# Kernel tuning notes

Measured on AMD Instinct MI355X. Metric: run time of the kernel, lower is better.

## Reference

```python
import jax, jax.numpy as jnp
import numpy as np

N_NODES = 25000
N_EDGES = 400000
N = 2          # per-node group dim (h.size(1))
IN_DIM = 64
HEADS = 4
HEAD_DIM = 16  # out_dim; HEADS*HEAD_DIM == IN_DIM here


def setup_inputs() -> dict:
    key = jax.random.key(0)
    ks = jax.random.split(key, 8)
    w_scale = 1.0 / np.sqrt(IN_DIM)
    return {
        "h": jax.random.normal(ks[0], (N_NODES, N, IN_DIM), jnp.float32),
        "e": jax.random.normal(ks[1], (N_EDGES, N, IN_DIM), jnp.float32),
        "W_Q": jax.random.normal(ks[2], (IN_DIM, HEADS * HEAD_DIM), jnp.float32) * w_scale,
        "W_K": jax.random.normal(ks[3], (IN_DIM, HEADS * HEAD_DIM), jnp.float32) * w_scale,
        "W_V": jax.random.normal(ks[4], (IN_DIM, HEADS * HEAD_DIM), jnp.float32) * w_scale,
        "W_repe": jax.random.normal(ks[5], (IN_DIM, HEADS * HEAD_DIM), jnp.float32) * w_scale,
        "src": jax.random.randint(ks[6], (N_EDGES,), 0, N_NODES, jnp.int32),
        "dst": jax.random.randint(ks[7], (N_EDGES,), 0, N_NODES, jnp.int32),
    }


def reference(h, e, W_Q, W_K, W_V, W_repe, src, dst):
    n_nodes, Nd, C = h.shape
    E = src.shape[0]
    # node-side projection Q_h: [n_nodes, N, H, D]
    Q_h = (h @ W_Q).reshape(n_nodes, Nd, HEADS, HEAD_DIM)
    # edge-side bias repe_e: [E, N, H, D]
    repe_e = (e @ W_repe).reshape(E, Nd, HEADS, HEAD_DIM)
    # compute_diff: relu(src - dst) on raw features  [E, N, C]
    diff = jax.nn.relu(h[src] - h[dst])
    k_diff = (diff @ W_K).reshape(E, Nd, HEADS, HEAD_DIM)
    v_diff = (diff @ W_V).reshape(E, Nd, HEADS, HEAD_DIM)
    # dst_cosim_diff: scale = ||k_diff|| * ||Q_h[dst]|| + 1e-6 (norm over last dim, keepdim)
    q_dst = Q_h[dst]  # [E, N, H, D]
    scale = (jnp.linalg.norm(k_diff, axis=-1, keepdims=True)
             * jnp.linalg.norm(q_dst, axis=-1, keepdims=True)) + 1e-6
    score = q_dst * k_diff * scale + repe_e
    msg = score * v_diff
    # update_all(copy_edge, max) -> segment max over dst; zero-degree nodes get 0 (DGL convention)
    h_out = jax.ops.segment_max(msg, dst, num_segments=n_nodes)
    h_out = jnp.where(jnp.isneginf(h_out), jnp.zeros((), h_out.dtype), h_out)
    return h_out
```

## Files before the change

kernel.cpp:

```cpp
#include <hip/hip_runtime.h>
#include <stdint.h>

#define N_NODES 25000
#define N_EDGES 400000

typedef __attribute__((ext_vector_type(8))) short short8;
typedef __attribute__((ext_vector_type(4))) float f32x4;

#define MFMA16(a, b, c) __builtin_amdgcn_mfma_f32_16x16x32_bf16((a), (b), (c), 0, 0, 0)

__device__ __forceinline__ short bf16r(float x) {
    unsigned u = __float_as_uint(x);
    u += 0x7FFFu + ((u >> 16) & 1u);
    return (short)(u >> 16);
}
__device__ __forceinline__ short bfr(float x) {
    return (short)((__float_as_uint(x) + 0x8000u) >> 16);
}

#define DPP_ADD(x, ctrl) \
    ((x) + __int_as_float(__builtin_amdgcn_update_dpp(0, __float_as_int(x), (ctrl), 0xF, 0xF, true)))
__device__ __forceinline__ float red16(float x) {
    x = DPP_ADD(x, 0xB1);
    x = DPP_ADD(x, 0x4E);
    x = DPP_ADD(x, 0x141);
    x = DPP_ADD(x, 0x140);
    return x;
}

__device__ __forceinline__ short8 load_bfrag(const float* __restrict__ W,
                                             int colbase, int lane, int khalf) {
    const int n = colbase + (lane & 15);
    const int k0 = khalf * 32 + ((lane >> 4) << 3);
    short8 f;
    #pragma unroll
    for (int j = 0; j < 8; ++j) f[j] = bf16r(W[(k0 + j) * 64 + n]);
    return f;
}

__device__ __forceinline__ short8 afrag(const short* S, int lane, int khalf) {
    return *(const short8*)&S[(lane & 15) * 72 + khalf * 32 + ((lane >> 4) << 3)];
}

__global__ __launch_bounds__(256) void zero_counts_kernel(int* __restrict__ counts) {
    const int i = blockIdx.x * 256 + threadIdx.x;
    if (i < N_NODES) counts[i] = 0;
}

__global__ __launch_bounds__(256) void hist_kernel(const int* __restrict__ dst,
                                                   int* __restrict__ counts) {
    const int i = blockIdx.x * 256 + threadIdx.x;
    if (i < N_EDGES) atomicAdd(&counts[dst[i]], 1);
}

#define BPT 98
__global__ __launch_bounds__(256) void scan_kernel(const int* __restrict__ counts,
                                                   int* __restrict__ offsets,
                                                   int* __restrict__ cursor) {
    __shared__ int part[256];
    const int t = threadIdx.x;
    const int base = t * BPT;
    int s = 0;
    for (int j = 0; j < BPT; ++j) {
        const int idx = base + j;
        if (idx < N_NODES) s += counts[idx];
    }
    part[t] = s;
    __syncthreads();
    for (int d = 1; d < 256; d <<= 1) {
        const int add = (t >= d) ? part[t - d] : 0;
        __syncthreads();
        part[t] += add;
        __syncthreads();
    }
    int run = (t > 0) ? part[t - 1] : 0;
    for (int j = 0; j < BPT; ++j) {
        const int idx = base + j;
        if (idx < N_NODES) {
            offsets[idx] = run;
            cursor[idx]  = run;
            run += counts[idx];
        }
    }
    if (t == 255) offsets[N_NODES] = part[255];
}

__global__ __launch_bounds__(256) void scatter_pos_kernel(
    const int* __restrict__ dst, int* __restrict__ cursor,
    int* __restrict__ csr_pos) {
    const int i = blockIdx.x * 256 + threadIdx.x;
    if (i < N_EDGES) {
        const int pos = atomicAdd(&cursor[dst[i]], 1);
        csr_pos[i] = pos;
    }
}

__global__ __launch_bounds__(256) void q_mfma_kernel(
    const float* __restrict__ h, const float* __restrict__ Wq,
    const float* __restrict__ Wk, const float* __restrict__ Wv,
    const float* __restrict__ Wr, float* __restrict__ Q, short8* __restrict__ fw)
{
    __shared__ short sH[64 * 72];
    const int t = threadIdx.x;
    const int lane = t & 63, w = t >> 6;
    const int wcol = w << 4;
    const int ln = lane & 15, lq = lane >> 4;
    const int base = blockIdx.x * 64;

    const short8 b0 = load_bfrag(Wq, wcol, lane, 0);
    const short8 b1 = load_bfrag(Wq, wcol, lane, 1);

    {
        const int r = t >> 2, c4 = (t & 3) << 4;
        int row = base + r; if (row > 49999) row = 49999;
        const float4* p = (const float4*)&h[row * 64 + c4];
        short tmp[16];
        #pragma unroll
        for (int i = 0; i < 4; ++i) {
            float4 x = p[i];
            tmp[4*i+0] = bf16r(x.x); tmp[4*i+1] = bf16r(x.y);
            tmp[4*i+2] = bf16r(x.z); tmp[4*i+3] = bf16r(x.w);
        }
        *(short8*)&sH[r * 72 + c4]     = *(short8*)&tmp[0];
        *(short8*)&sH[r * 72 + c4 + 8] = *(short8*)&tmp[8];
    }
    __syncthreads();

    #pragma unroll
    for (int m = 0; m < 4; ++m) {
        const short* Sm = &sH[(m << 4) * 72];
        short8 a0 = afrag(Sm, lane, 0);
        short8 a1 = afrag(Sm, lane, 1);
        f32x4 acc = {0.f, 0.f, 0.f, 0.f};
        acc = MFMA16(a0, b0, acc);
        acc = MFMA16(a1, b1, acc);
        #pragma unroll
        for (int reg = 0; reg < 4; ++reg) {
            const float qn = sqrtf(red16(acc[reg] * acc[reg]));
            const int row = base + (m << 4) + (lq << 2) + reg;
            if (row < 50000) Q[row * 64 + wcol + ln] = acc[reg] * qn;
        }
    }

    if (blockIdx.x == 0) {
        fw[(w * 6 + 0) * 64 + lane] = load_bfrag(Wk, wcol, lane, 0);
        fw[(w * 6 + 1) * 64 + lane] = load_bfrag(Wk, wcol, lane, 1);
        fw[(w * 6 + 2) * 64 + lane] = load_bfrag(Wv, wcol, lane, 0);
        fw[(w * 6 + 3) * 64 + lane] = load_bfrag(Wv, wcol, lane, 1);
        fw[(w * 6 + 4) * 64 + lane] = load_bfrag(Wr, wcol, lane, 0);
        fw[(w * 6 + 5) * 64 + lane] = load_bfrag(Wr, wcol, lane, 1);
    }
}

__global__ __launch_bounds__(256, 4) void edge_msg_kernel(
    const float* __restrict__ h, const float* __restrict__ e,
    const float* __restrict__ QQ, const int* __restrict__ src,
    const int* __restrict__ dst, const int* __restrict__ csr_pos,
    const short8* __restrict__ fw, uint2* __restrict__ msg)
{
    const int t = threadIdx.x;
    const int lane = t & 63;
    const int g = (blockIdx.x << 2) + (t >> 6);
    const int g8 = g << 3;
    const int ln = lane & 15, lq = lane >> 4;
    const int eloc = ln >> 1, nr = ln & 1;
    const int k0 = lq << 3;

    const int sA = src[g8 + eloc];
    const int dA = dst[g8 + eloc];
    const float* __restrict__ hs  = &h[((sA << 1) + nr) << 6];
    const float* __restrict__ hdp = &h[((dA << 1) + nr) << 6];
    const float* __restrict__ ep  = &e[(((g8 + eloc) << 1) + nr) << 6];

    short8 afr[2], gfr[2];
    #pragma unroll
    for (int half = 0; half < 2; ++half) {
        const int cb = (half << 5) + k0;
        const float4 s0 = *(const float4*)&hs[cb];
        const float4 s1 = *(const float4*)&hs[cb + 4];
        const float4 d0 = *(const float4*)&hdp[cb];
        const float4 d1 = *(const float4*)&hdp[cb + 4];
        const float4 e0 = *(const float4*)&ep[cb];
        const float4 e1 = *(const float4*)&ep[cb + 4];
        short8 ta, tg;
        ta[0] = bfr(fmaxf(s0.x - d0.x, 0.f));
        ta[1] = bfr(fmaxf(s0.y - d0.y, 0.f));
        ta[2] = bfr(fmaxf(s0.z - d0.z, 0.f));
        ta[3] = bfr(fmaxf(s0.w - d0.w, 0.f));
        ta[4] = bfr(fmaxf(s1.x - d1.x, 0.f));
        ta[5] = bfr(fmaxf(s1.y - d1.y, 0.f));
        ta[6] = bfr(fmaxf(s1.z - d1.z, 0.f));
        ta[7] = bfr(fmaxf(s1.w - d1.w, 0.f));
        tg[0] = bfr(e0.x); tg[1] = bfr(e0.y); tg[2] = bfr(e0.z); tg[3] = bfr(e0.w);
        tg[4] = bfr(e1.x); tg[5] = bfr(e1.y); tg[6] = bfr(e1.z); tg[7] = bfr(e1.w);
        afr[half] = ta;
        gfr[half] = tg;
    }

    const int e0i = g8 + (lq << 1), e1i = e0i + 1;
    const int d0 = dst[e0i], d1 = dst[e1i];
    const int p0 = csr_pos[e0i], p1 = csr_pos[e1i];

    float qv_e0n0[4], qv_e0n1[4], qv_e1n0[4], qv_e1n1[4];
    #pragma unroll
    for (int hd = 0; hd < 4; ++hd) {
        qv_e0n0[hd] = QQ[(d0 << 7) + (hd << 4) + ln];
        qv_e0n1[hd] = QQ[(d0 << 7) + 64 + (hd << 4) + ln];
        qv_e1n0[hd] = QQ[(d1 << 7) + (hd << 4) + ln];
        qv_e1n1[hd] = QQ[(d1 << 7) + 64 + (hd << 4) + ln];
    }

    f32x4 aK[4], aV[4], aR[4];
    #pragma unroll
    for (int hd = 0; hd < 4; ++hd) {
        f32x4 k = {0.f, 0.f, 0.f, 0.f}, vv = k, r = k;
        k  = MFMA16(afr[0], fw[(hd * 6 + 0) * 64 + lane], k);
        k  = MFMA16(afr[1], fw[(hd * 6 + 1) * 64 + lane], k);
        vv = MFMA16(afr[0], fw[(hd * 6 + 2) * 64 + lane], vv);
        vv = MFMA16(afr[1], fw[(hd * 6 + 3) * 64 + lane], vv);
        r  = MFMA16(gfr[0], fw[(hd * 6 + 4) * 64 + lane], r);
        r  = MFMA16(gfr[1], fw[(hd * 6 + 5) * 64 + lane], r);
        aK[hd] = k; aV[hd] = vv; aR[hd] = r;
    }

    #pragma unroll
    for (int reg = 0; reg < 4; ++reg) {
        float m[4];
        #pragma unroll
        for (int hd = 0; hd < 4; ++hd) {
            const float kk = aK[hd][reg];
            const float nk = sqrtf(red16(kk * kk));
            const float qv = (reg == 0) ? qv_e0n0[hd] :
                             (reg == 1) ? qv_e0n1[hd] :
                             (reg == 2) ? qv_e1n0[hd] : qv_e1n1[hd];
            m[hd] = (qv * kk * nk + aR[hd][reg]) * aV[hd][reg];
        }
        uint2 pk;
        pk.x = (unsigned)(unsigned short)bf16r(m[0])
             | ((unsigned)(unsigned short)bf16r(m[1]) << 16);
        pk.y = (unsigned)(unsigned short)bf16r(m[2])
             | ((unsigned)(unsigned short)bf16r(m[3]) << 16);
        const int p = (reg & 2) ? p1 : p0;
        msg[(((p << 1) + (reg & 1)) << 4) + ln] = pk;
    }
}

__global__ __launch_bounds__(256) void reduce_kernel(
    const unsigned* __restrict__ msg_u, const int* __restrict__ offsets,
    float* __restrict__ out)
{
    const int t = threadIdx.x;
    const int lane = t & 63;
    const int v = (blockIdx.x << 2) + (t >> 6);
    const int off0 = offsets[v], off1 = offsets[v + 1];
    const int n = lane >> 5, ph = (lane >> 4) & 1, ln = lane & 15;
    const unsigned* __restrict__ p = msg_u + ((n << 5) + (ln << 1) + ph);

    const float NEG_INF = __uint_as_float(0xFF800000u);
    float m0 = NEG_INF, m1 = NEG_INF;

    int pos = off0;
    for (; pos + 4 <= off1; pos += 4) {
        const unsigned u0 = p[(pos + 0) << 6];
        const unsigned u1 = p[(pos + 1) << 6];
        const unsigned u2 = p[(pos + 2) << 6];
        const unsigned u3 = p[(pos + 3) << 6];
        m0 = fmaxf(m0, __uint_as_float(u0 << 16));
        m1 = fmaxf(m1, __uint_as_float(u0 & 0xFFFF0000u));
        m0 = fmaxf(m0, __uint_as_float(u1 << 16));
        m1 = fmaxf(m1, __uint_as_float(u1 & 0xFFFF0000u));
        m0 = fmaxf(m0, __uint_as_float(u2 << 16));
        m1 = fmaxf(m1, __uint_as_float(u2 & 0xFFFF0000u));
        m0 = fmaxf(m0, __uint_as_float(u3 << 16));
        m1 = fmaxf(m1, __uint_as_float(u3 & 0xFFFF0000u));
    }
    for (; pos < off1; ++pos) {
        const unsigned u = p[pos << 6];
        m0 = fmaxf(m0, __uint_as_float(u << 16));
        m1 = fmaxf(m1, __uint_as_float(u & 0xFFFF0000u));
    }
    if (off0 == off1) { m0 = 0.f; m1 = 0.f; }

    const int col = (n << 6) + (ph << 5) + ln;
    out[(v << 7) + col]      = m0;
    out[(v << 7) + col + 16] = m1;
}

extern "C" void kernel_launch(void* const* d_in, const int* in_sizes, int n_in,
                              void* d_out, int out_size, void* d_ws, size_t ws_size,
                              hipStream_t stream) {
    const float* h  = (const float*)d_in[0];
    const float* e  = (const float*)d_in[1];
    const float* Wq = (const float*)d_in[2];
    const float* Wk = (const float*)d_in[3];
    const float* Wv = (const float*)d_in[4];
    const float* Wr = (const float*)d_in[5];
    const int*   src = (const int*)d_in[6];
    const int*   dst = (const int*)d_in[7];
    float* out = (float*)d_out;

    float* Q       = (float*)d_ws;
    int*   counts  = (int*)d_ws + 3200000;
    int*   offsets = (int*)d_ws + 3225000;
    int*   cursor  = (int*)d_ws + 3250008;
    int*   csr_pos = (int*)d_ws + 3275008;
    short8* fw     = (short8*)((int*)d_ws + 3675008);
    uint2* msg     = (uint2*)((int*)d_ws + 3681152);

    zero_counts_kernel<<<98, 256, 0, stream>>>(counts);
    hist_kernel<<<1563, 256, 0, stream>>>(dst, counts);
    scan_kernel<<<1, 256, 0, stream>>>(counts, offsets, cursor);
    scatter_pos_kernel<<<1563, 256, 0, stream>>>(dst, cursor, csr_pos);
    q_mfma_kernel<<<782, 256, 0, stream>>>(h, Wq, Wk, Wv, Wr, Q, fw);
    edge_msg_kernel<<<12500, 256, 0, stream>>>(h, e, Q, src, dst, csr_pos, fw, msg);
    reduce_kernel<<<6250, 256, 0, stream>>>((const unsigned*)msg, offsets, out);
}
```

Before: 534.9 us.

## Replace CSR segment-max with atomicMax on order-mapped floats and bf16 node buffer

```diff
diff --git a/kernel.cpp b/kernel.cpp
--- a/kernel.cpp
+++ b/kernel.cpp
@@ -28,6 +28,25 @@
     return x;
 }
 
+__device__ __forceinline__ unsigned fmap(float x) {
+    const unsigned u = __float_as_uint(x);
+    return ((int)u >= 0) ? (u | 0x80000000u) : ~u;
+}
+#define MAPPED_NEG_INF 0x007FFFFFu
+
+__device__ __forceinline__ float pickbf(unsigned u, int odd) {
+    return __uint_as_float(odd ? (u & 0xFFFF0000u) : (u << 16));
+}
+__device__ __forceinline__ unsigned drelu_pack(unsigned s, unsigned d) {
+    const float slo = __uint_as_float(s << 16);
+    const float shi = __uint_as_float(s & 0xFFFF0000u);
+    const float dlo = __uint_as_float(d << 16);
+    const float dhi = __uint_as_float(d & 0xFFFF0000u);
+    const unsigned lo = (unsigned short)bfr(fmaxf(slo - dlo, 0.f));
+    const unsigned hi = (unsigned short)bfr(fmaxf(shi - dhi, 0.f));
+    return lo | (hi << 16);
+}
+
 __device__ __forceinline__ short8 load_bfrag(const float* __restrict__ W,
                                              int colbase, int lane, int khalf) {
     const int n = colbase + (lane & 15);
@@ -42,63 +61,15 @@
     return *(const short8*)&S[(lane & 15) * 72 + khalf * 32 + ((lane >> 4) << 3)];
 }
 
-__global__ __launch_bounds__(256) void zero_counts_kernel(int* __restrict__ counts) {
+__global__ __launch_bounds__(256) void init_kernel(unsigned* __restrict__ out_u) {
     const int i = blockIdx.x * 256 + threadIdx.x;
-    if (i < N_NODES) counts[i] = 0;
-}
-
-__global__ __launch_bounds__(256) void hist_kernel(const int* __restrict__ dst,
-                                                   int* __restrict__ counts) {
-    const int i = blockIdx.x * 256 + threadIdx.x;
-    if (i < N_EDGES) atomicAdd(&counts[dst[i]], 1);
-}
-
-#define BPT 98
-__global__ __launch_bounds__(256) void scan_kernel(const int* __restrict__ counts,
-                                                   int* __restrict__ offsets,
-                                                   int* __restrict__ cursor) {
-    __shared__ int part[256];
-    const int t = threadIdx.x;
-    const int base = t * BPT;
-    int s = 0;
-    for (int j = 0; j < BPT; ++j) {
-        const int idx = base + j;
-        if (idx < N_NODES) s += counts[idx];
-    }
-    part[t] = s;
-    __syncthreads();
-    for (int d = 1; d < 256; d <<= 1) {
-        const int add = (t >= d) ? part[t - d] : 0;
-        __syncthreads();
-        part[t] += add;
-        __syncthreads();
-    }
-    int run = (t > 0) ? part[t - 1] : 0;
-    for (int j = 0; j < BPT; ++j) {
-        const int idx = base + j;
-        if (idx < N_NODES) {
-            offsets[idx] = run;
-            cursor[idx]  = run;
-            run += counts[idx];
-        }
-    }
-    if (t == 255) offsets[N_NODES] = part[255];
-}
-
-__global__ __launch_bounds__(256) void scatter_pos_kernel(
-    const int* __restrict__ dst, int* __restrict__ cursor,
-    int* __restrict__ csr_pos) {
-    const int i = blockIdx.x * 256 + threadIdx.x;
-    if (i < N_EDGES) {
-        const int pos = atomicAdd(&cursor[dst[i]], 1);
-        csr_pos[i] = pos;
-    }
+    out_u[i] = MAPPED_NEG_INF;
 }
 
 __global__ __launch_bounds__(256) void q_mfma_kernel(
     const float* __restrict__ h, const float* __restrict__ Wq,
     const float* __restrict__ Wk, const float* __restrict__ Wv,
-    const float* __restrict__ Wr, float* __restrict__ Q, short8* __restrict__ fw)
+    const float* __restrict__ Wr, unsigned* __restrict__ NB, short8* __restrict__ fw)
 {
     __shared__ short sH[64 * 72];
     const int t = threadIdx.x;
@@ -123,6 +94,9 @@
         }
         *(short8*)&sH[r * 72 + c4]     = *(short8*)&tmp[0];
         *(short8*)&sH[r * 72 + c4 + 8] = *(short8*)&tmp[8];
+        unsigned* nb = NB + ((row >> 1) << 7) + ((row & 1) << 5) + (c4 >> 1);
+        *(short8*)(nb)     = *(short8*)&tmp[0];
+        *(short8*)(nb + 4) = *(short8*)&tmp[8];
     }
     __syncthreads();
 
@@ -137,8 +111,14 @@
         #pragma unroll
         for (int reg = 0; reg < 4; ++reg) {
             const float qn = sqrtf(red16(acc[reg] * acc[reg]));
+            const float qq = acc[reg] * qn;
+            const float qo = __shfl_xor(qq, 1);
             const int row = base + (m << 4) + (lq << 2) + reg;
-            if (row < 50000) Q[row * 64 + wcol + ln] = acc[reg] * qn;
+            if (((ln & 1) == 0) && row < 50000) {
+                const unsigned u = (unsigned)(unsigned short)bf16r(qq)
+                                 | ((unsigned)(unsigned short)bf16r(qo) << 16);
+                NB[((row >> 1) << 7) + 64 + ((row & 1) << 5) + (w << 3) + (ln >> 1)] = u;
+            }
         }
     }
 
@@ -152,11 +132,10 @@
     }
 }
 
-__global__ __launch_bounds__(256, 4) void edge_msg_kernel(
-    const float* __restrict__ h, const float* __restrict__ e,
-    const float* __restrict__ QQ, const int* __restrict__ src,
-    const int* __restrict__ dst, const int* __restrict__ csr_pos,
-    const short8* __restrict__ fw, uint2* __restrict__ msg)
+__global__ __launch_bounds__(256, 4) void edge_atomic_kernel(
+    const float* __restrict__ e, const int* __restrict__ src,
+    const int* __restrict__ dst, const unsigned* __restrict__ NB,
+    const short8* __restrict__ fw, unsigned* __restrict__ out_u)
 {
     const int t = threadIdx.x;
     const int lane = t & 63;
@@ -168,122 +147,88 @@
 
     const int sA = src[g8 + eloc];
     const int dA = dst[g8 + eloc];
-    const float* __restrict__ hs  = &h[((sA << 1) + nr) << 6];
-    const float* __restrict__ hdp = &h[((dA << 1) + nr) << 6];
-    const float* __restrict__ ep  = &e[(((g8 + eloc) << 1) + nr) << 6];
-
-    short8 afr[2], gfr[2];
+    const unsigned* nbs = NB + (sA << 7) + (nr << 5);
+    const unsigned* nbd = NB + (dA << 7) + (nr << 5);
+    const uint4 su0 = ((const uint4*)nbs)[lq];
+    const uint4 su1 = ((const uint4*)nbs)[4 + lq];
+    const uint4 du0 = ((const uint4*)nbd)[lq];
+    const uint4 du1 = ((const uint4*)nbd)[4 + lq];
+    uint4 a0u, a1u;
+    a0u.x = drelu_pack(su0.x, du0.x); a0u.y = drelu_pack(su0.y, du0.y);
+    a0u.z = drelu_pack(su0.z, du0.z); a0u.w = drelu_pack(su0.w, du0.w);
+    a1u.x = drelu_pack(su1.x, du1.x); a1u.y = drelu_pack(su1.y, du1.y);
+    a1u.z = drelu_pack(su1.z, du1.z); a1u.w = drelu_pack(su1.w, du1.w);
+    const short8 afr0 = *(const short8*)&a0u;
+    const short8 afr1 = *(const short8*)&a1u;
+
+    const float* __restrict__ ep = &e[(((g8 + eloc) << 1) + nr) << 6];
+    short8 gfr0, gfr1;
     #pragma unroll
     for (int half = 0; half < 2; ++half) {
         const int cb = (half << 5) + k0;
-        const float4 s0 = *(const float4*)&hs[cb];
-        const float4 s1 = *(const float4*)&hs[cb + 4];
-        const float4 d0 = *(const float4*)&hdp[cb];
-        const float4 d1 = *(const float4*)&hdp[cb + 4];
         const float4 e0 = *(const float4*)&ep[cb];
         const float4 e1 = *(const float4*)&ep[cb + 4];
-        short8 ta, tg;
-        ta[0] = bfr(fmaxf(s0.x - d0.x, 0.f));
-        ta[1] = bfr(fmaxf(s0.y - d0.y, 0.f));
-        ta[2] = bfr(fmaxf(s0.z - d0.z, 0.f));
-        ta[3] = bfr(fmaxf(s0.w - d0.w, 0.f));
-        ta[4] = bfr(fmaxf(s1.x - d1.x, 0.f));
-        ta[5] = bfr(fmaxf(s1.y - d1.y, 0.f));
-        ta[6] = bfr(fmaxf(s1.z - d1.z, 0.f));
-        ta[7] = bfr(fmaxf(s1.w - d1.w, 0.f));
+        short8 tg;
         tg[0] = bfr(e0.x); tg[1] = bfr(e0.y); tg[2] = bfr(e0.z); tg[3] = bfr(e0.w);
         tg[4] = bfr(e1.x); tg[5] = bfr(e1.y); tg[6] = bfr(e1.z); tg[7] = bfr(e1.w);
-        afr[half] = ta;
-        gfr[half] = tg;
+        if (half == 0) gfr0 = tg; else gfr1 = tg;
     }
 
     const int e0i = g8 + (lq << 1), e1i = e0i + 1;
     const int d0 = dst[e0i], d1 = dst[e1i];
-    const int p0 = csr_pos[e0i], p1 = csr_pos[e1i];
-
-    float qv_e0n0[4], qv_e0n1[4], qv_e1n0[4], qv_e1n1[4];
+
+    const unsigned* q0p = NB + (d0 << 7) + 64 + (ln >> 1);
+    const unsigned* q1p = NB + (d1 << 7) + 64 + (ln >> 1);
+    float qvr[4][4];
     #pragma unroll
     for (int hd = 0; hd < 4; ++hd) {
-        qv_e0n0[hd] = QQ[(d0 << 7) + (hd << 4) + ln];
-        qv_e0n1[hd] = QQ[(d0 << 7) + 64 + (hd << 4) + ln];
-        qv_e1n0[hd] = QQ[(d1 << 7) + (hd << 4) + ln];
-        qv_e1n1[hd] = QQ[(d1 << 7) + 64 + (hd << 4) + ln];
+        qvr[0][hd] = pickbf(q0p[hd << 3],        ln & 1);
+        qvr[1][hd] = pickbf(q0p[32 + (hd << 3)], ln & 1);
+        qvr[2][hd] = pickbf(q1p[hd << 3],        ln & 1);
+        qvr[3][hd] = pickbf(q1p[32 + (hd << 3)], ln & 1);
     }
 
     f32x4 aK[4], aV[4], aR[4];
     #pragma unroll
     for (int hd = 0; hd < 4; ++hd) {
         f32x4 k = {0.f, 0.f, 0.f, 0.f}, vv = k, r = k;
-        k  = MFMA16(afr[0], fw[(hd * 6 + 0) * 64 + lane], k);
-        k  = MFMA16(afr[1], fw[(hd * 6 + 1) * 64 + lane], k);
-        vv = MFMA16(afr[0], fw[(hd * 6 + 2) * 64 + lane], vv);
-        vv = MFMA16(afr[1], fw[(hd * 6 + 3) * 64 + lane], vv);
-        r  = MFMA16(gfr[0], fw[(hd * 6 + 4) * 64 + lane], r);
-        r  = MFMA16(gfr[1], fw[(hd * 6 + 5) * 64 + lane], r);
+        k  = MFMA16(afr0, fw[(hd * 6 + 0) * 64 + lane], k);
+        k  = MFMA16(afr1, fw[(hd * 6 + 1) * 64 + lane], k);
+        vv = MFMA16(afr0, fw[(hd * 6 + 2) * 64 + lane], vv);
+        vv = MFMA16(afr1, fw[(hd * 6 + 3) * 64 + lane], vv);
+        r  = MFMA16(gfr0, fw[(hd * 6 + 4) * 64 + lane], r);
+        r  = MFMA16(gfr1, fw[(hd * 6 + 5) * 64 + lane], r);
         aK[hd] = k; aV[hd] = vv; aR[hd] = r;
     }
 
     #pragma unroll
     for (int reg = 0; reg < 4; ++reg) {
-        float m[4];
+        unsigned* ob = out_u + (((reg & 2) ? d1 : d0) << 7) + ((reg & 1) << 6) + ln;
         #pragma unroll
         for (int hd = 0; hd < 4; ++hd) {
             const float kk = aK[hd][reg];
             const float nk = sqrtf(red16(kk * kk));
-            const float qv = (reg == 0) ? qv_e0n0[hd] :
-                             (reg == 1) ? qv_e0n1[hd] :
-                             (reg == 2) ? qv_e1n0[hd] : qv_e1n1[hd];
-            m[hd] = (qv * kk * nk + aR[hd][reg]) * aV[hd][reg];
+            const float m = (qvr[reg][hd] * kk * nk + aR[hd][reg]) * aV[hd][reg];
+            atomicMax(ob + (hd << 4), fmap(m));
         }
-        uint2 pk;
-        pk.x = (unsigned)(unsigned short)bf16r(m[0])
-             | ((unsigned)(unsigned short)bf16r(m[1]) << 16);
-        pk.y = (unsigned)(unsigned short)bf16r(m[2])
-             | ((unsigned)(unsigned short)bf16r(m[3]) << 16);
-        const int p = (reg & 2) ? p1 : p0;
-        msg[(((p << 1) + (reg & 1)) << 4) + ln] = pk;
-    }
-}
-
-__global__ __launch_bounds__(256) void reduce_kernel(
-    const unsigned* __restrict__ msg_u, const int* __restrict__ offsets,
-    float* __restrict__ out)
-{
-    const int t = threadIdx.x;
-    const int lane = t & 63;
-    const int v = (blockIdx.x << 2) + (t >> 6);
-    const int off0 = offsets[v], off1 = offsets[v + 1];
-    const int n = lane >> 5, ph = (lane >> 4) & 1, ln = lane & 15;
-    const unsigned* __restrict__ p = msg_u + ((n << 5) + (ln << 1) + ph);
-
-    const float NEG_INF = __uint_as_float(0xFF800000u);
-    float m0 = NEG_INF, m1 = NEG_INF;
-
-    int pos = off0;
-    for (; pos + 4 <= off1; pos += 4) {
-        const unsigned u0 = p[(pos + 0) << 6];
-        const unsigned u1 = p[(pos + 1) << 6];
-        const unsigned u2 = p[(pos + 2) << 6];
-        const unsigned u3 = p[(pos + 3) << 6];
-        m0 = fmaxf(m0, __uint_as_float(u0 << 16));
-        m1 = fmaxf(m1, __uint_as_float(u0 & 0xFFFF0000u));
-        m0 = fmaxf(m0, __uint_as_float(u1 << 16));
-        m1 = fmaxf(m1, __uint_as_float(u1 & 0xFFFF0000u));
-        m0 = fmaxf(m0, __uint_as_float(u2 << 16));
-        m1 = fmaxf(m1, __uint_as_float(u2 & 0xFFFF0000u));
-        m0 = fmaxf(m0, __uint_as_float(u3 << 16));
-        m1 = fmaxf(m1, __uint_as_float(u3 & 0xFFFF0000u));
-    }
-    for (; pos < off1; ++pos) {
-        const unsigned u = p[pos << 6];
-        m0 = fmaxf(m0, __uint_as_float(u << 16));
-        m1 = fmaxf(m1, __uint_as_float(u & 0xFFFF0000u));
-    }
-    if (off0 == off1) { m0 = 0.f; m1 = 0.f; }
-
-    const int col = (n << 6) + (ph << 5) + ln;
-    out[(v << 7) + col]      = m0;
-    out[(v << 7) + col + 16] = m1;
+    }
+}
+
+__global__ __launch_bounds__(256) void final_kernel(unsigned* __restrict__ io) {
+    const int i = blockIdx.x * 256 + threadIdx.x;
+    uint4* p = (uint4*)io;
+    uint4 m = p[i];
+    unsigned a, b, c, d;
+    a = (m.x & 0x80000000u) ? (m.x ^ 0x80000000u) : ~m.x;
+    b = (m.y & 0x80000000u) ? (m.y ^ 0x80000000u) : ~m.y;
+    c = (m.z & 0x80000000u) ? (m.z ^ 0x80000000u) : ~m.z;
+    d = (m.w & 0x80000000u) ? (m.w ^ 0x80000000u) : ~m.w;
+    if (a == 0xFF800000u) a = 0u;
+    if (b == 0xFF800000u) b = 0u;
+    if (c == 0xFF800000u) c = 0u;
+    if (d == 0xFF800000u) d = 0u;
+    m.x = a; m.y = b; m.z = c; m.w = d;
+    p[i] = m;
 }
 
 extern "C" void kernel_launch(void* const* d_in, const int* in_sizes, int n_in,
@@ -299,19 +244,11 @@
     const int*   dst = (const int*)d_in[7];
     float* out = (float*)d_out;
 
-    float* Q       = (float*)d_ws;
-    int*   counts  = (int*)d_ws + 3200000;
-    int*   offsets = (int*)d_ws + 3225000;
-    int*   cursor  = (int*)d_ws + 3250008;
-    int*   csr_pos = (int*)d_ws + 3275008;
-    short8* fw     = (short8*)((int*)d_ws + 3675008);
-    uint2* msg     = (uint2*)((int*)d_ws + 3681152);
-
-    zero_counts_kernel<<<98, 256, 0, stream>>>(counts);
-    hist_kernel<<<1563, 256, 0, stream>>>(dst, counts);
-    scan_kernel<<<1, 256, 0, stream>>>(counts, offsets, cursor);
-    scatter_pos_kernel<<<1563, 256, 0, stream>>>(dst, cursor, csr_pos);
-    q_mfma_kernel<<<782, 256, 0, stream>>>(h, Wq, Wk, Wv, Wr, Q, fw);
-    edge_msg_kernel<<<12500, 256, 0, stream>>>(h, e, Q, src, dst, csr_pos, fw, msg);
-    reduce_kernel<<<6250, 256, 0, stream>>>((const unsigned*)msg, offsets, out);
-}
+    unsigned* NB = (unsigned*)d_ws;
+    short8*   fw = (short8*)((int*)d_ws + 3200000);
+
+    init_kernel<<<12500, 256, 0, stream>>>((unsigned*)out);
+    q_mfma_kernel<<<782, 256, 0, stream>>>(h, Wq, Wk, Wv, Wr, NB, fw);
+    edge_atomic_kernel<<<12500, 256, 0, stream>>>(e, src, dst, NB, fw, (unsigned*)out);
+    final_kernel<<<3125, 256, 0, stream>>>((unsigned*)out);
+}
```

New measurement: 439.5 us. 17.8% less time.
